# Performance work log

Hardware: AMD Instinct MI355X
Metric: run time of the kernel (lower is better)

## Reference

```python
import jax, jax.numpy as jnp
import numpy as np
from jax import lax

EMBED = 512
HIDDEN = 1024
VOCAB = 50257
BATCH = 64


def setup_inputs() -> dict:
    key = jax.random.key(0)
    ks = jax.random.split(key, 7)
    s_ih = 1.0 / np.sqrt(HIDDEN)
    inp = {
        "features": jax.random.normal(ks[0], (BATCH, EMBED), dtype=jnp.float32),
        "W_ih": jax.random.uniform(ks[1], (4 * HIDDEN, EMBED), jnp.float32, -s_ih, s_ih),
        "W_hh": jax.random.uniform(ks[2], (4 * HIDDEN, HIDDEN), jnp.float32, -s_ih, s_ih),
        "b_ih": jax.random.uniform(ks[3], (4 * HIDDEN,), jnp.float32, -s_ih, s_ih),
        "b_hh": jax.random.uniform(ks[4], (4 * HIDDEN,), jnp.float32, -s_ih, s_ih),
        "W_fc": jax.random.uniform(ks[5], (VOCAB, HIDDEN), jnp.float32, -s_ih, s_ih),
        "b_fc": jax.random.uniform(ks[6], (VOCAB,), jnp.float32, -s_ih, s_ih),
        "max_seq_len": 18,
    }
    return inp


def reference(features, W_ih, W_hh, b_ih, b_hh, W_fc, b_fc, max_seq_len):
    # features: [B, E] fed at EVERY step (module re-feeds the same features).
    B = features.shape[0]
    H = W_hh.shape[1]
    # Input projection is constant across steps; hoist it (same math).
    x_proj = features @ W_ih.T + b_ih  # [B, 4H]

    def step(carry, _):
        h, c = carry
        gates = x_proj + h @ W_hh.T + b_hh  # [B, 4H], PyTorch gate order i,f,g,o
        i, f, g, o = jnp.split(gates, 4, axis=1)
        i = jax.nn.sigmoid(i)
        f = jax.nn.sigmoid(f)
        g = jnp.tanh(g)
        o = jax.nn.sigmoid(o)
        c_new = f * c + i * g
        h_new = o * jnp.tanh(c_new)
        out = h_new @ W_fc.T + b_fc  # [B, V]
        return (h_new, c_new), out

    h0 = jnp.zeros((B, H), dtype=features.dtype)
    c0 = jnp.zeros((B, H), dtype=features.dtype)
    _, outs = lax.scan(step, (h0, c0), None, length=max_seq_len)  # [T, B, V]
    return jnp.transpose(outs, (1, 0, 2))  # [B, T, V]
```

## Files before the change

kernel.cpp:

```cpp
#include <hip/hip_runtime.h>

#define EMBED  512
#define HIDDEN 1024
#define G4     4096
#define VOCAB  50257
#define BATCH  64
#define TSTEPS 18
#define MROWS  (BATCH*TSTEPS)

typedef __bf16 bf16x8 __attribute__((ext_vector_type(8)));
typedef float  f32x4  __attribute__((ext_vector_type(4)));

#define WS_HA_B   0
#define WS_HB_B   131072
#define WS_BAR_B  262144
#define WS_XB_B   524288
#define WS_HS_B   1572864

#define NLSTM_BLK 64

__device__ inline bf16x8 cvt2bf8(float4 a, float4 b) {
    bf16x8 v;
    v[0] = (__bf16)a.x; v[1] = (__bf16)a.y; v[2] = (__bf16)a.z; v[3] = (__bf16)a.w;
    v[4] = (__bf16)b.x; v[5] = (__bf16)b.y; v[6] = (__bf16)b.z; v[7] = (__bf16)b.w;
    return v;
}

__global__ __launch_bounds__(256) void k_xproj(const float* __restrict__ feat,
                                               const float* __restrict__ W_ih,
                                               const float* __restrict__ b_ih,
                                               const float* __restrict__ b_hh,
                                               float* __restrict__ xb,
                                               unsigned* __restrict__ flags) {
    if (blockIdx.x == 0 && blockIdx.y == 0) {
        #pragma unroll
        for (int k = 0; k < 8; ++k) flags[threadIdx.x * 8 + k] = 0u;
    }
    __shared__ float fsh[16][EMBED];
    const int tx = threadIdx.x;
    const int rc = blockIdx.x;
    const int b0 = blockIdx.y * 16;
    {
        int row = tx >> 4, seg = tx & 15;
        const float4* src = (const float4*)(feat + (b0 + row) * EMBED + seg * 32);
        float4* dst = (float4*)(&fsh[row][seg * 32]);
        #pragma unroll
        for (int c = 0; c < 8; ++c) dst[c] = src[c];
    }
    __syncthreads();
    const int jl = tx & 15, bl = tx >> 4;
    const int r = rc * 16 + jl;
    const int b = b0 + bl;
    const float4* w  = (const float4*)(W_ih + (size_t)r * EMBED);
    const float4* h4 = (const float4*)(&fsh[bl][0]);
    float acc = 0.f;
    #pragma unroll 4
    for (int k = 0; k < EMBED / 4; ++k) {
        float4 wv = w[k], hv = h4[k];
        acc += wv.x * hv.x + wv.y * hv.y + wv.z * hv.z + wv.w * hv.w;
    }
    xb[b * G4 + r] = acc + b_ih[r] + b_hh[r];
}

__device__ __forceinline__ void store_h_sc(__bf16* p, __bf16 v) {
    unsigned hv = (unsigned)__builtin_bit_cast(unsigned short, v);
    asm volatile("global_store_short %0, %1, off sc0 sc1" :: "v"(p), "v"(hv) : "memory");
}

#define WAIT0 asm volatile("s_waitcnt vmcnt(0)" ::: "memory")
#define WAIT4 asm volatile("s_waitcnt vmcnt(4)" ::: "memory")
#define SBAR  __builtin_amdgcn_sched_barrier(0)

__device__ __forceinline__ void step_barrier(unsigned* flags, int bid, int wave,
                                             int lane, unsigned t) {
    WAIT0;
    __syncthreads();
    if (threadIdx.x == 0) {
        unsigned* fp = flags + (size_t)bid * 32;
        asm volatile("global_store_dword %0, %1, off sc0 sc1" :: "v"(fp), "v"(t) : "memory");
    }
    if (wave == 0) {
        const unsigned* pp = flags + (size_t)lane * 32;
        unsigned v;
        for (;;) {
            asm volatile("global_load_dword %0, %1, off sc0 sc1\n\t"
                         "s_waitcnt vmcnt(0)"
                         : "=&v"(v) : "v"(pp) : "memory");
            if (__all((int)(v >= t))) break;
            __builtin_amdgcn_s_sleep(1);
        }
    }
    __syncthreads();
}

#define PJT 17

#define LOADS(dst, sidx) do {                                                   \
    const int _ko = (sidx) * 32;                                                \
    _Pragma("unroll")                                                           \
    for (int _i = 0; _i < 4; ++_i) {                                            \
        const __bf16* _p = aBase + (size_t)_i * 16 * HIDDEN + _ko;              \
        asm volatile("global_load_dwordx4 %0, %1, off sc0 sc1"                  \
                     : "=&v"(dst[_i]) : "v"(_p) : "memory");                    \
    } } while (0)

#define MFMAS(src, sidx) do {                                                   \
    _Pragma("unroll")                                                           \
    for (int _i = 0; _i < 4; ++_i)                                              \
        _Pragma("unroll")                                                       \
        for (int _g = 0; _g < 4; ++_g)                                          \
            acc[_i][_g] = __builtin_amdgcn_mfma_f32_16x16x32_bf16(              \
                src[_i], bB[_g][sidx], acc[_i][_g], 0, 0, 0);                   \
    } while (0)

__global__ __launch_bounds__(256, 1) void k_lstm(const float* __restrict__ xb,
                                                 const float* __restrict__ Whh32,
                                                 __bf16* __restrict__ hA,
                                                 __bf16* __restrict__ hB,
                                                 __bf16* __restrict__ hs,
                                                 unsigned* __restrict__ flags) {
    __shared__ float part[16 * 64 * PJT];
    const int tx   = threadIdx.x;
    const int wave = tx >> 6;
    const int lane = tx & 63;
    const int q    = lane >> 4;
    const int r    = lane & 15;
    const int bid  = blockIdx.x;
    const int j0   = bid * 16;
    const int kb   = wave * 256;

    bf16x8 bB[4][8];
    {
        const float* bsrc = Whh32 + (size_t)(j0 + r) * HIDDEN + kb + q * 8;
        #pragma unroll
        for (int g = 0; g < 4; ++g)
            #pragma unroll
            for (int s = 0; s < 8; ++s) {
                const float4* p = (const float4*)(bsrc + (size_t)g * 1024 * HIDDEN + s * 32);
                bB[g][s] = cvt2bf8(p[0], p[1]);
            }
    }

    const int jl = tx & 15;
    const int m0 = tx >> 4;
    float cr[4];
    float xbr[4][4];
    #pragma unroll
    for (int mi = 0; mi < 4; ++mi) {
        cr[mi] = 0.f;
        const int m = mi * 16 + m0;
        #pragma unroll
        for (int g = 0; g < 4; ++g)
            xbr[mi][g] = xb[m * G4 + g * 1024 + j0 + jl];
    }

    #pragma unroll
    for (int mi = 0; mi < 4; ++mi) {
        const int m = mi * 16 + m0;
        const float i_ = 1.f / (1.f + expf(-xbr[mi][0]));
        const float g_ = tanhf(xbr[mi][2]);
        const float o_ = 1.f / (1.f + expf(-xbr[mi][3]));
        const float cn = i_ * g_;
        cr[mi] = cn;
        const float hn = o_ * tanhf(cn);
        const __bf16 hb = (__bf16)hn;
        store_h_sc(hB + m * HIDDEN + j0 + jl, hb);
        hs[(size_t)(m * TSTEPS + 0) * HIDDEN + j0 + jl] = hb;
    }

    #pragma unroll 1
    for (int t = 1; t < TSTEPS; ++t) {
        step_barrier(flags, bid, wave, lane, (unsigned)t);
        const __bf16* hi = (t & 1) ? hB : hA;
        __bf16*       ho = (t & 1) ? hA : hB;

        f32x4 acc[4][4];
        #pragma unroll
        for (int i = 0; i < 4; ++i)
            #pragma unroll
            for (int g = 0; g < 4; ++g)
                acc[i][g] = (f32x4){0.f, 0.f, 0.f, 0.f};

        const __bf16* aBase = hi + (size_t)r * HIDDEN + kb + q * 8;
        bf16x8 avA[4], avB[4];

        LOADS(avA, 0);
        LOADS(avB, 1);
        WAIT4; SBAR; MFMAS(avA, 0);
        LOADS(avA, 2);
        WAIT4; SBAR; MFMAS(avB, 1);
        LOADS(avB, 3);
        WAIT4; SBAR; MFMAS(avA, 2);
        LOADS(avA, 4);
        WAIT4; SBAR; MFMAS(avB, 3);
        LOADS(avB, 5);
        WAIT4; SBAR; MFMAS(avA, 4);
        LOADS(avA, 6);
        WAIT4; SBAR; MFMAS(avB, 5);
        LOADS(avB, 7);
        WAIT4; SBAR; MFMAS(avA, 6);
        WAIT0; SBAR; MFMAS(avB, 7);

        #pragma unroll
        for (int i = 0; i < 4; ++i)
            #pragma unroll
            for (int g = 0; g < 4; ++g)
                #pragma unroll
                for (int reg = 0; reg < 4; ++reg)
                    part[((wave * 4 + g) * 64 + i * 16 + q * 4 + reg) * PJT + r] = acc[i][g][reg];
        __syncthreads();

        #pragma unroll
        for (int mi = 0; mi < 4; ++mi) {
            const int m = mi * 16 + m0;
            float gsum[4];
            #pragma unroll
            for (int g = 0; g < 4; ++g) {
                float s = xbr[mi][g];
                #pragma unroll
                for (int w = 0; w < 4; ++w)
                    s += part[((w * 4 + g) * 64 + m) * PJT + jl];
                gsum[g] = s;
            }
            const float i_ = 1.f / (1.f + expf(-gsum[0]));
            const float f_ = 1.f / (1.f + expf(-gsum[1]));
            const float g_ = tanhf(gsum[2]);
            const float o_ = 1.f / (1.f + expf(-gsum[3]));
            const float cn = f_ * cr[mi] + i_ * g_;
            cr[mi] = cn;
            const float hn = o_ * tanhf(cn);
            const __bf16 hb = (__bf16)hn;
            store_h_sc(ho + m * HIDDEN + j0 + jl, hb);
            hs[(size_t)(m * TSTEPS + t) * HIDDEN + j0 + jl] = hb;
        }
        __syncthreads();
    }
}

#define LPITCH 40
#define NBLK 393
#define MBLK 9
#define NWG  (NBLK*MBLK)
#define XQ   (NWG/8)
#define XR   (NWG%8)

__global__ __launch_bounds__(256) void k_fc(const __bf16* __restrict__ hs,
                                            const float* __restrict__ W_fc,
                                            const float* __restrict__ b_fc,
                                            float* __restrict__ out) {
    __shared__ __bf16 Ash[128 * LPITCH];
    __shared__ __bf16 Bsh[128 * LPITCH];
    const int tx = threadIdx.x;
    const int bid = blockIdx.x;
    const int xcd = bid & 7;
    const int lid = bid >> 3;
    const int base = (xcd < XR) ? xcd * (XQ + 1) : XR * (XQ + 1) + (xcd - XR) * XQ;
    const int virt = base + lid;
    const int mb = (virt % MBLK) * 128;
    const int nb = (virt / MBLK) * 128;

    const int srow = tx >> 1;
    const int half = tx & 1;
    const __bf16* aSrc = hs + (size_t)(mb + srow) * HIDDEN + half * 16;
    const int nclamp = min(nb + srow, VOCAB - 1);
    const float4* bSrc = (const float4*)(W_fc + (size_t)nclamp * HIDDEN + half * 16);
    __bf16* aDst = &Ash[srow * LPITCH + half * 16];
    __bf16* bDst = &Bsh[srow * LPITCH + half * 16];

    const int lane = tx & 63;
    const int wave = tx >> 6;
    const int q = lane >> 4;
    const int r = lane & 15;
    const int wm = (wave >> 1) * 64;
    const int wn = (wave & 1) * 64;

    const __bf16* aF[4];
    const __bf16* bF[4];
    #pragma unroll
    for (int i = 0; i < 4; ++i) aF[i] = &Ash[(wm + i * 16 + r) * LPITCH + q * 8];
    #pragma unroll
    for (int j = 0; j < 4; ++j) bF[j] = &Bsh[(wn + j * 16 + r) * LPITCH + q * 8];

    f32x4 acc[4][4];
    #pragma unroll
    for (int i = 0; i < 4; ++i)
        #pragma unroll
        for (int j = 0; j < 4; ++j)
            acc[i][j] = (f32x4){0.f, 0.f, 0.f, 0.f};

    bf16x8 a0p = *(const bf16x8*)aSrc;
    bf16x8 a1p = *(const bf16x8*)(aSrc + 8);
    float4 f0p = bSrc[0], f1p = bSrc[1], f2p = bSrc[2], f3p = bSrc[3];
    aSrc += 32; bSrc += 8;

    for (int k0 = 0; k0 < HIDDEN; k0 += 32) {
        *(bf16x8*)aDst = a0p;
        *(bf16x8*)(aDst + 8) = a1p;
        *(bf16x8*)bDst = cvt2bf8(f0p, f1p);
        *(bf16x8*)(bDst + 8) = cvt2bf8(f2p, f3p);
        __syncthreads();
        if (k0 + 32 < HIDDEN) {
            a0p = *(const bf16x8*)aSrc;
            a1p = *(const bf16x8*)(aSrc + 8);
            f0p = bSrc[0]; f1p = bSrc[1]; f2p = bSrc[2]; f3p = bSrc[3];
            aSrc += 32; bSrc += 8;
        }
        bf16x8 av[4], bv[4];
        #pragma unroll
        for (int i = 0; i < 4; ++i) av[i] = *(const bf16x8*)aF[i];
        #pragma unroll
        for (int j = 0; j < 4; ++j) bv[j] = *(const bf16x8*)bF[j];
        #pragma unroll
        for (int i = 0; i < 4; ++i)
            #pragma unroll
            for (int j = 0; j < 4; ++j)
                acc[i][j] = __builtin_amdgcn_mfma_f32_16x16x32_bf16(av[i], bv[j], acc[i][j], 0, 0, 0);
        __syncthreads();
    }

    #pragma unroll
    for (int j = 0; j < 4; ++j) {
        const int v = nb + wn + j * 16 + r;
        if (v < VOCAB) {
            const float bias = b_fc[v];
            #pragma unroll
            for (int i = 0; i < 4; ++i) {
                const int m0 = mb + wm + i * 16 + q * 4;
                float* op = out + (size_t)m0 * VOCAB + v;
                op[0]                 = acc[i][j][0] + bias;
                op[(size_t)VOCAB]     = acc[i][j][1] + bias;
                op[(size_t)VOCAB * 2] = acc[i][j][2] + bias;
                op[(size_t)VOCAB * 3] = acc[i][j][3] + bias;
            }
        }
    }
}

extern "C" void kernel_launch(void* const* d_in, const int* in_sizes, int n_in,
                              void* d_out, int out_size, void* d_ws, size_t ws_size,
                              hipStream_t stream) {
    const float* feat = (const float*)d_in[0];
    const float* W_ih = (const float*)d_in[1];
    const float* W_hh = (const float*)d_in[2];
    const float* b_ih = (const float*)d_in[3];
    const float* b_hh = (const float*)d_in[4];
    const float* W_fc = (const float*)d_in[5];
    const float* b_fc = (const float*)d_in[6];
    float* out = (float*)d_out;

    char* wsb = (char*)d_ws;
    __bf16*   hA    = (__bf16*)(wsb + WS_HA_B);
    __bf16*   hB    = (__bf16*)(wsb + WS_HB_B);
    unsigned* flags = (unsigned*)(wsb + WS_BAR_B);
    float*    xb    = (float*)(wsb + WS_XB_B);
    __bf16*   hs    = (__bf16*)(wsb + WS_HS_B);

    k_xproj<<<dim3(256, 4), 256, 0, stream>>>(feat, W_ih, b_ih, b_hh, xb, flags);
    k_lstm<<<NLSTM_BLK, 256, 0, stream>>>(xb, W_hh, hA, hB, hs, flags);
    k_fc<<<NWG, 256, 0, stream>>>(hs, W_fc, b_fc, out);
}
```

Measured before the change: 814.6 us.

## Double-buffer FC GEMM with BK=64, swizzled LDS, and coalesced LDS-staged epilogue

Reworks the vocabulary projection GEMM to use a K-tile of 64 with double-buffered shared memory, so there is one barrier per tile and global loads for the next tile overlap the MFMAs. Uses an XOR-style slot swizzle in place of row padding to avoid LDS bank conflicts. The epilogue stages accumulators through shared memory so each wave writes contiguous rows of the output, replacing the strided 4-row scatter stores. The cost is 64 KB of LDS per block, which lowers occupancy, plus extra barriers in the epilogue.

```diff
diff --git a/kernel.cpp b/kernel.cpp
--- a/kernel.cpp
+++ b/kernel.cpp
@@ -237,7 +237,7 @@
     }
 }
 
-#define LPITCH 40
+#define BKF  64
 #define NBLK 393
 #define MBLK 9
 #define NWG  (NBLK*MBLK)
@@ -248,9 +248,12 @@
                                             const float* __restrict__ W_fc,
                                             const float* __restrict__ b_fc,
                                             float* __restrict__ out) {
-    __shared__ __bf16 Ash[128 * LPITCH];
-    __shared__ __bf16 Bsh[128 * LPITCH];
-    const int tx = threadIdx.x;
+    __shared__ __align__(16) char smem[65536];
+    __bf16* As = (__bf16*)smem;
+    __bf16* Bs = (__bf16*)(smem + 32768);
+    float*  Ct = (float*)smem;
+
+    const int tx  = threadIdx.x;
     const int bid = blockIdx.x;
     const int xcd = bid & 7;
     const int lid = bid >> 3;
@@ -259,14 +262,6 @@
     const int mb = (virt % MBLK) * 128;
     const int nb = (virt / MBLK) * 128;
 
-    const int srow = tx >> 1;
-    const int half = tx & 1;
-    const __bf16* aSrc = hs + (size_t)(mb + srow) * HIDDEN + half * 16;
-    const int nclamp = min(nb + srow, VOCAB - 1);
-    const float4* bSrc = (const float4*)(W_fc + (size_t)nclamp * HIDDEN + half * 16);
-    __bf16* aDst = &Ash[srow * LPITCH + half * 16];
-    __bf16* bDst = &Bsh[srow * LPITCH + half * 16];
-
     const int lane = tx & 63;
     const int wave = tx >> 6;
     const int q = lane >> 4;
@@ -274,12 +269,34 @@
     const int wm = (wave >> 1) * 64;
     const int wn = (wave & 1) * 64;
 
-    const __bf16* aF[4];
-    const __bf16* bF[4];
-    #pragma unroll
-    for (int i = 0; i < 4; ++i) aF[i] = &Ash[(wm + i * 16 + r) * LPITCH + q * 8];
-    #pragma unroll
-    for (int j = 0; j < 4; ++j) bF[j] = &Bsh[(wn + j * 16 + r) * LPITCH + q * 8];
+    const int srow = tx >> 1;
+    const int half = tx & 1;
+    const __bf16* aSrc = hs + (size_t)(mb + srow) * HIDDEN + half * 32;
+    const int nclamp = min(nb + srow, VOCAB - 1);
+    const float* bSrc = W_fc + (size_t)nclamp * HIDDEN + half * 32;
+    __bf16* aD = As + srow * BKF;
+    __bf16* bD = Bs + srow * BKF;
+
+    bf16x8 aR[4];
+    float4 bR[8];
+
+#define FC_LOAD(k0) do {                                                        \
+    _Pragma("unroll")                                                           \
+    for (int cc = 0; cc < 4; ++cc)                                              \
+        aR[cc] = *(const bf16x8*)(aSrc + (k0) + cc * 8);                        \
+    _Pragma("unroll")                                                           \
+    for (int cc = 0; cc < 8; ++cc)                                              \
+        bR[cc] = *(const float4*)(bSrc + (k0) + cc * 4);                        \
+} while (0)
+
+#define FC_STAGE(buf) do {                                                      \
+    _Pragma("unroll")                                                           \
+    for (int cc = 0; cc < 4; ++cc) {                                            \
+        const int slot = (half * 4 + cc + srow) & 7;                            \
+        *(bf16x8*)(aD + (buf) * 8192 + slot * 8) = aR[cc];                      \
+        *(bf16x8*)(bD + (buf) * 8192 + slot * 8) = cvt2bf8(bR[cc*2], bR[cc*2+1]); \
+    }                                                                           \
+} while (0)
 
     f32x4 acc[4][4];
     #pragma unroll
@@ -288,52 +305,65 @@
         for (int j = 0; j < 4; ++j)
             acc[i][j] = (f32x4){0.f, 0.f, 0.f, 0.f};
 
-    bf16x8 a0p = *(const bf16x8*)aSrc;
-    bf16x8 a1p = *(const bf16x8*)(aSrc + 8);
-    float4 f0p = bSrc[0], f1p = bSrc[1], f2p = bSrc[2], f3p = bSrc[3];
-    aSrc += 32; bSrc += 8;
-
-    for (int k0 = 0; k0 < HIDDEN; k0 += 32) {
-        *(bf16x8*)aDst = a0p;
-        *(bf16x8*)(aDst + 8) = a1p;
-        *(bf16x8*)bDst = cvt2bf8(f0p, f1p);
-        *(bf16x8*)(bDst + 8) = cvt2bf8(f2p, f3p);
-        __syncthreads();
-        if (k0 + 32 < HIDDEN) {
-            a0p = *(const bf16x8*)aSrc;
-            a1p = *(const bf16x8*)(aSrc + 8);
-            f0p = bSrc[0]; f1p = bSrc[1]; f2p = bSrc[2]; f3p = bSrc[3];
-            aSrc += 32; bSrc += 8;
+    FC_LOAD(0);
+    FC_STAGE(0);
+    __syncthreads();
+
+    for (int kt = 0; kt < 16; ++kt) {
+        const int cur = kt & 1;
+        if (kt < 15) FC_LOAD((kt + 1) * BKF);
+        const __bf16* Ab = As + cur * 8192;
+        const __bf16* Bb = Bs + cur * 8192;
+        #pragma unroll
+        for (int kk = 0; kk < 2; ++kk) {
+            bf16x8 av[4], bv[4];
+            #pragma unroll
+            for (int i = 0; i < 4; ++i) {
+                const int row = wm + i * 16 + r;
+                av[i] = *(const bf16x8*)(Ab + row * BKF + ((kk * 4 + q + row) & 7) * 8);
+            }
+            #pragma unroll
+            for (int j = 0; j < 4; ++j) {
+                const int row = wn + j * 16 + r;
+                bv[j] = *(const bf16x8*)(Bb + row * BKF + ((kk * 4 + q + row) & 7) * 8);
+            }
+            #pragma unroll
+            for (int i = 0; i < 4; ++i)
+                #pragma unroll
+                for (int j = 0; j < 4; ++j)
+                    acc[i][j] = __builtin_amdgcn_mfma_f32_16x16x32_bf16(av[i], bv[j], acc[i][j], 0, 0, 0);
         }
-        bf16x8 av[4], bv[4];
-        #pragma unroll
-        for (int i = 0; i < 4; ++i) av[i] = *(const bf16x8*)aF[i];
-        #pragma unroll
-        for (int j = 0; j < 4; ++j) bv[j] = *(const bf16x8*)bF[j];
-        #pragma unroll
-        for (int i = 0; i < 4; ++i)
-            #pragma unroll
-            for (int j = 0; j < 4; ++j)
-                acc[i][j] = __builtin_amdgcn_mfma_f32_16x16x32_bf16(av[i], bv[j], acc[i][j], 0, 0, 0);
-        __syncthreads();
-    }
+        if (kt < 15) FC_STAGE(cur ^ 1);
+        __syncthreads();
+    }
+
+    const int v0 = nb + lane;
+    const int v1 = nb + 64 + lane;
+    float bias0 = 0.f, bias1 = 0.f;
+    if (v0 < VOCAB) bias0 = b_fc[v0];
+    if (v1 < VOCAB) bias1 = b_fc[v1];
 
     #pragma unroll
-    for (int j = 0; j < 4; ++j) {
-        const int v = nb + wn + j * 16 + r;
-        if (v < VOCAB) {
-            const float bias = b_fc[v];
-            #pragma unroll
-            for (int i = 0; i < 4; ++i) {
-                const int m0 = mb + wm + i * 16 + q * 4;
-                float* op = out + (size_t)m0 * VOCAB + v;
-                op[0]                 = acc[i][j][0] + bias;
-                op[(size_t)VOCAB]     = acc[i][j][1] + bias;
-                op[(size_t)VOCAB * 2] = acc[i][j][2] + bias;
-                op[(size_t)VOCAB * 3] = acc[i][j][3] + bias;
-            }
+    for (int i = 0; i < 4; ++i) {
+        #pragma unroll
+        for (int j = 0; j < 4; ++j)
+            #pragma unroll
+            for (int reg = 0; reg < 4; ++reg)
+                Ct[((wave >> 1) * 16 + q * 4 + reg) * 128 + wn + j * 16 + r] = acc[i][j][reg];
+        __syncthreads();
+        #pragma unroll
+        for (int rr8 = 0; rr8 < 8; ++rr8) {
+            const int rr = wave * 8 + rr8;
+            const int m = mb + ((rr < 16) ? (i * 16 + rr) : (48 + i * 16 + rr));
+            const float cA = Ct[rr * 128 + lane];
+            const float cB = Ct[rr * 128 + 64 + lane];
+            if (v0 < VOCAB) out[(size_t)m * VOCAB + v0] = cA + bias0;
+            if (v1 < VOCAB) out[(size_t)m * VOCAB + v1] = cB + bias1;
         }
-    }
+        __syncthreads();
+    }
+#undef FC_LOAD
+#undef FC_STAGE
 }
 
 extern "C" void kernel_launch(void* const* d_in, const int* in_sizes, int n_in,
```

Result: slower. 912.1 us (+12.0%).
